# Kernel optimization log

Hardware: AMD Instinct MI355X
Metric: run time of the kernel (lower is better)

The kernel has to match this reference:

```python
import jax, jax.numpy as jnp
import numpy as np

HEADS = 4


def rel_to_abs(x):
    """Convert relative logits [..., L, 2L-1] to absolute [..., L, L].
    out[..., i, j] = x[..., i, j - i + L - 1]."""
    L = x.shape[-2]
    idx = jnp.arange(L)[None, :] - jnp.arange(L)[:, None] + (L - 1)  # [L, L]
    idx = jnp.broadcast_to(idx, x.shape[:-1] + (L,))
    return jnp.take_along_axis(x, idx, axis=-1)


def setup_inputs() -> dict:
    key = jax.random.key(0)
    ks = jax.random.split(key, 5)
    b, c, h, w = 2, 256, 64, 64
    dh = c // HEADS
    return {
        "x": jax.random.normal(ks[0], (b, c, h, w), jnp.float32),
        "w_qkv": jax.random.normal(ks[1], (3 * c, c), jnp.float32) / np.float32(np.sqrt(c)),
        "w_out": jax.random.normal(ks[2], (c, c), jnp.float32) / np.float32(np.sqrt(c)),
        "rel_height": jax.random.normal(ks[3], (2 * h - 1, dh), jnp.float32),
        "rel_width": jax.random.normal(ks[4], (2 * w - 1, dh), jnp.float32),
    }


def reference(x, w_qkv, w_out, rel_height, rel_width):
    b, c, h, w = x.shape
    dh = c // HEADS
    N = h * w
    scale = dh ** -0.5

    # 1x1 conv == per-pixel matmul over channels
    qkv = jnp.einsum('bchw,oc->bohw', x, w_qkv)  # [b, 3c, h, w]
    q, k, v = jnp.split(qkv, 3, axis=1)

    def to_heads(t):  # [b, c, h, w] -> [b, H, N, dh]
        return t.reshape(b, HEADS, dh, N).transpose(0, 1, 3, 2)

    q = to_heads(q) * scale
    k = to_heads(k)
    v = to_heads(v)

    # content-content scores over spatial positions
    content = jnp.einsum('bnid,bnjd->bnij', q, k)  # [b, H, N, N]

    q5 = q.reshape(b, HEADS, h, w, dh)  # [b, H, x, y, dh]
    # width relative logits: [b,H,x,y,2w-1] -> abs -> [b,H,x,y,jw]
    rw = rel_to_abs(jnp.einsum('bnxyd,rd->bnxyr', q5, rel_width))
    # height relative logits on transposed spatial: [b,H,y,x,2h-1] -> [b,H,y,x,jh]
    rh = rel_to_abs(jnp.einsum('bnyxd,rd->bnyxr', q5.transpose(0, 1, 3, 2, 4), rel_height))

    logits = content.reshape(b, HEADS, h, w, h, w)
    logits = logits + rw[:, :, :, :, None, :]  # broadcast width bias over target height jh
    logits = logits + rh.transpose(0, 1, 3, 2, 4)[:, :, :, :, :, None]  # [b,H,x,y,jh] over jw

    attn = jax.nn.softmax(logits.reshape(b, HEADS, N, N), axis=-1)
    out = jnp.einsum('bnij,bnjd->bnid', attn, v)  # [b, H, N, dh]
    out = out.transpose(0, 1, 3, 2).reshape(b, c, h, w)
    out = jnp.einsum('bchw,oc->bohw', out, w_out)  # 1x1 out projection
    return out + x
```

## Files before the change

kernel.cpp:

```cpp
#include <hip/hip_runtime.h>

typedef unsigned short u16;
typedef unsigned int u32;
typedef __bf16 bf16x8 __attribute__((ext_vector_type(8)));
typedef __bf16 bf16x2 __attribute__((ext_vector_type(2)));
typedef float f32x4 __attribute__((ext_vector_type(4)));
typedef float f32x2 __attribute__((ext_vector_type(2)));
typedef u32 u32x4 __attribute__((ext_vector_type(4)));
typedef u32 u32x2 __attribute__((ext_vector_type(2)));
typedef short s16x4 __attribute__((ext_vector_type(4)));

#define DEVI __device__ __forceinline__

#if defined(__has_builtin)
#if __has_builtin(__builtin_amdgcn_exp2f)
#define EXP2F(x) __builtin_amdgcn_exp2f(x)
#endif
#endif
#ifndef EXP2F
#define EXP2F(x) exp2f(x)
#endif

#define MFMA16(a, b, c) __builtin_amdgcn_mfma_f32_16x16x32_bf16(a, b, c, 0, 0, 0)
#define MFMA1K(a, b, c) __builtin_amdgcn_mfma_f32_16x16x16bf16_1k(a, b, c, 0, 0, 0)

typedef __attribute__((address_space(1))) u32 gu32;
typedef __attribute__((address_space(3))) u32 lu32;
DEVI void gll16(const u16* g, u16* l) {
    __builtin_amdgcn_global_load_lds((const gu32*)g, (lu32*)l, 16, 0, 0);
}
#define WAIT_VM0() __builtin_amdgcn_s_waitcnt(0x0f70)

DEVI u16 f2bf(float f) {
    u32 u = __builtin_bit_cast(u32, f);
    u = (u + 0x7FFFu + ((u >> 16) & 1u)) >> 16;
    return (u16)u;
}
DEVI float bf2f(u16 h) {
    u32 u = ((u32)h) << 16;
    return __builtin_bit_cast(float, u);
}
DEVI float bfhi(u32 u) { return __builtin_bit_cast(float, u & 0xFFFF0000u); }
DEVI float bflo(u32 u) { return __builtin_bit_cast(float, u << 16); }
DEVI bf16x8 bc8(u32x4 u) { return __builtin_bit_cast(bf16x8, u); }
DEVI s16x4 bc4(u32 a, u32 b) {
    u32x2 v = {a, b};
    return __builtin_bit_cast(s16x4, v);
}
DEVI u32 pack2(float a, float b) {
    f32x2 v = {a, b};
    bf16x2 h = __builtin_convertvector(v, bf16x2);
    return __builtin_bit_cast(u32, h);
}

#define QSCALE 0.18033688011112042f

__global__ __launch_bounds__(256) void k_prep(const float* __restrict__ x,
                                              const float* __restrict__ wq,
                                              const float* __restrict__ wo,
                                              const float* __restrict__ relh,
                                              const float* __restrict__ relw,
                                              u16* __restrict__ xt, u16* __restrict__ wqb,
                                              u16* __restrict__ wob, u16* __restrict__ relhb,
                                              u16* __restrict__ relwb) {
    int bid = blockIdx.x;
    int t = threadIdx.x;
    if (bid < 512) {
        int pm = bid & 63, cm = (bid >> 6) & 3, b = bid >> 8;
        int p0 = pm * 64, c0 = cm * 64;
        __shared__ float tile[64][65];
#pragma unroll
        for (int it = 0; it < 4; ++it) {
            int idx = it * 256 + t;
            int cl = idx >> 4, f4 = idx & 15;
            f32x4 v = *(const f32x4*)(x + ((size_t)(b * 256 + c0 + cl)) * 4096 + p0 + f4 * 4);
            tile[cl][f4 * 4 + 0] = v[0];
            tile[cl][f4 * 4 + 1] = v[1];
            tile[cl][f4 * 4 + 2] = v[2];
            tile[cl][f4 * 4 + 3] = v[3];
        }
        __syncthreads();
#pragma unroll
        for (int it = 0; it < 2; ++it) {
            int idx = it * 256 + t;
            int pl = idx >> 3, g = idx & 7;
            u32x4 pk;
            pk.x = pack2(tile[g * 8 + 0][pl], tile[g * 8 + 1][pl]);
            pk.y = pack2(tile[g * 8 + 2][pl], tile[g * 8 + 3][pl]);
            pk.z = pack2(tile[g * 8 + 4][pl], tile[g * 8 + 5][pl]);
            pk.w = pack2(tile[g * 8 + 6][pl], tile[g * 8 + 7][pl]);
            *(u32x4*)(xt + ((size_t)(b * 4096 + p0 + pl)) * 256 + c0 + g * 8) = pk;
        }
    } else {
        int i0 = (bid - 512) * 256 + t;
#pragma unroll
        for (int i = i0; i < 196608; i += 65536) wqb[i] = f2bf(wq[i]);
        if (i0 < 65536) wob[i0] = f2bf(wo[i0]);
        if (i0 < 8192) {
            relhb[i0] = (i0 < 8128) ? f2bf(relh[i0]) : (u16)0;
            relwb[i0] = (i0 < 8128) ? f2bf(relw[i0]) : (u16)0;
        }
    }
}

__global__ __launch_bounds__(256) void k_qkv(const u16* __restrict__ xt, const u16* __restrict__ wqb,
                                             const u16* __restrict__ relwb,
                                             const u16* __restrict__ relhb,
                                             u16* __restrict__ q, u16* __restrict__ k,
                                             u16* __restrict__ vt, u16* __restrict__ Wabs,
                                             u16* __restrict__ HabsT) {
    int pm = blockIdx.x, on = blockIdx.y, b = blockIdx.z;
    int p0 = pm * 64, o0 = on * 64;
    __shared__ __align__(16) u16 Sm[64 * 256];
    int t = threadIdx.x;
    int wv = t >> 6, l = t & 63, quad = l >> 4, li = l & 15;

    u32x4 areg[8];
    const u32x4* arow = (const u32x4*)(xt + ((size_t)(b * 4096 + p0 + wv * 16 + li)) * 256);
#pragma unroll
    for (int kc = 0; kc < 8; ++kc) areg[kc] = arow[kc * 4 + quad];

    {
        int pc = l & 31;
#pragma unroll
        for (int i = 0; i < 8; ++i) {
            int r = wv * 16 + i * 2 + (l >> 5);
            gll16(wqb + (size_t)(o0 + r) * 256 + ((pc + r) & 31) * 8,
                  Sm + (wv * 16 + i * 2) * 256);
        }
    }
    WAIT_VM0();
    __syncthreads();

    f32x4 acc[4] = {{0, 0, 0, 0}, {0, 0, 0, 0}, {0, 0, 0, 0}, {0, 0, 0, 0}};
#pragma unroll
    for (int kc = 0; kc < 8; ++kc) {
        bf16x8 a = bc8(areg[kc]);
#pragma unroll
        for (int ct = 0; ct < 4; ++ct) {
            bf16x8 bb = bc8(*(const u32x4*)(Sm + (ct * 16 + li) * 256 +
                                            (((kc * 4 + quad) - (ct * 16 + li)) & 31) * 8));
            acc[ct] = MFMA16(a, bb, acc[ct]);
        }
    }

    int tensor = on >> 2, head = on & 3;
    if (tensor == 2) {
        __syncthreads();
        u16* T = Sm;
#pragma unroll
        for (int ct = 0; ct < 4; ++ct)
#pragma unroll
            for (int r = 0; r < 4; ++r)
                T[(ct * 16 + li) * 72 + wv * 16 + quad * 4 + r] = f2bf(acc[ct][r]);
        __syncthreads();
        int dr = t >> 2, pc = (t & 3) * 16;
        u32x4* g = (u32x4*)(vt + ((size_t)((b * 4 + head) * 64 + dr)) * 4096 + p0 + pc);
        const u32x4* s2 = (const u32x4*)(T + dr * 72 + pc);
        g[0] = s2[0];
        g[1] = s2[1];
    } else {
        u16* outp = (tensor == 0) ? q : k;
        float sc = (tensor == 0) ? QSCALE : 1.0f;
#pragma unroll
        for (int ct = 0; ct < 4; ++ct)
#pragma unroll
            for (int r = 0; r < 4; ++r) {
                int p = p0 + wv * 16 + quad * 4 + r;
                int d = ct * 16 + li;
                outp[((size_t)((b * 4 + head) * 4096 + p)) * 64 + d] = f2bf(acc[ct][r] * sc);
            }
        if (tensor == 0) {
            int bh = b * 4 + head;
            u16* T = Sm;
            u16* Ls = Sm + 64 * 72;
            __syncthreads();
#pragma unroll
            for (int ct = 0; ct < 4; ++ct)
#pragma unroll
                for (int r = 0; r < 4; ++r)
                    T[(wv * 16 + quad * 4 + r) * 72 + ct * 16 + li] = f2bf(acc[ct][r] * QSCALE);
            {
                int row = t >> 1, half = t & 1;
                const u32x4* g2 = (const u32x4*)(relwb + row * 64 + half * 32);
                u32x4* s2 = (u32x4*)(Ls + row * 72 + half * 32);
#pragma unroll
                for (int kk = 0; kk < 4; ++kk) s2[kk] = g2[kk];
            }
            __syncthreads();
            u32x4 aq2[2];
            aq2[0] = *(const u32x4*)(T + (wv * 16 + li) * 72 + quad * 8);
            aq2[1] = *(const u32x4*)(T + (wv * 16 + li) * 72 + 32 + quad * 8);

            f32x4 acc2[8];
#pragma unroll
            for (int ct = 0; ct < 8; ++ct) acc2[ct] = (f32x4){0.f, 0.f, 0.f, 0.f};
#pragma unroll
            for (int kc = 0; kc < 2; ++kc) {
                bf16x8 a = bc8(aq2[kc]);
#pragma unroll
                for (int ct = 0; ct < 8; ++ct) {
                    bf16x8 bb = bc8(*(const u32x4*)(Ls + (ct * 16 + li) * 72 + kc * 32 + quad * 8));
                    acc2[ct] = MFMA16(a, bb, acc2[ct]);
                }
            }
#pragma unroll
            for (int ct = 0; ct < 8; ++ct)
#pragma unroll
                for (int r = 0; r < 4; ++r) {
                    int row = wv * 16 + quad * 4 + r;
                    int j = (ct * 16 + li) - 63 + row;
                    if (j >= 0 && j < 64)
                        Wabs[((size_t)(bh * 4096 + p0 + row)) * 64 + j] = f2bf(acc2[ct][r]);
                }
            __syncthreads();
            {
                int row = t >> 1, half = t & 1;
                const u32x4* g2 = (const u32x4*)(relhb + row * 64 + half * 32);
                u32x4* s2 = (u32x4*)(Ls + row * 72 + half * 32);
#pragma unroll
                for (int kk = 0; kk < 4; ++kk) s2[kk] = g2[kk];
            }
            __syncthreads();
#pragma unroll
            for (int ct = 0; ct < 8; ++ct) acc2[ct] = (f32x4){0.f, 0.f, 0.f, 0.f};
#pragma unroll
            for (int kc = 0; kc < 2; ++kc) {
                bf16x8 a = bc8(aq2[kc]);
#pragma unroll
                for (int ct = 0; ct < 8; ++ct) {
                    bf16x8 bb = bc8(*(const u32x4*)(Ls + (ct * 16 + li) * 72 + kc * 32 + quad * 8));
                    acc2[ct] = MFMA16(a, bb, acc2[ct]);
                }
            }
#pragma unroll
            for (int ct = 0; ct < 8; ++ct)
#pragma unroll
                for (int r = 0; r < 4; ++r) {
                    int row = wv * 16 + quad * 4 + r;
                    int j = (ct * 16 + li) - 63 + pm;
                    if (j >= 0 && j < 64)
                        HabsT[((size_t)(bh * 64 + j)) * 4096 + p0 + row] = f2bf(acc2[ct][r]);
                }
        }
    }
}

__global__ __launch_bounds__(256, 2) void k_flash(const u16* __restrict__ q,
                                                  const u16* __restrict__ kg,
                                                  const u16* __restrict__ vt,
                                                  const u16* __restrict__ Wabs,
                                                  const u16* __restrict__ HabsT,
                                                  u16* __restrict__ OP,
                                                  float* __restrict__ LS) {
    int pm = blockIdx.x, bh = blockIdx.y, ks = blockIdx.z;
    int p0 = pm * 128;
    __shared__ __align__(16) u16 Kt[2][64 * 72];
    __shared__ __align__(16) u16 Vl[2][64 * 72];
    int t = threadIdx.x, wv = t >> 6, l = t & 63, quad = l >> 4, li = l & 15;
    int rbase = wv * 32;

    u32x4 aq[2][2];
#pragma unroll
    for (int rs = 0; rs < 2; ++rs) {
        const u32x4* qrow =
            (const u32x4*)(q + ((size_t)(bh * 4096 + p0 + rbase + rs * 16 + li)) * 64);
        aq[rs][0] = qrow[quad];
        aq[rs][1] = qrow[4 + quad];
    }

    f32x4 wb4[2][4];
#pragma unroll
    for (int rs = 0; rs < 2; ++rs)
#pragma unroll
        for (int ct = 0; ct < 4; ++ct) {
            const u32* wp = (const u32*)(Wabs +
                                         ((size_t)(bh * 4096 + p0 + rbase + rs * 16 + li)) * 64 +
                                         ct * 16 + quad * 4);
            u32 lo = wp[0], hi = wp[1];
            wb4[rs][ct] = (f32x4){bflo(lo), bfhi(lo), bflo(hi), bfhi(hi)};
        }

    const u16* hbase = HabsT + ((size_t)(bh * 64 + ks * 32)) * 4096 + p0 + rbase;

    int srow = t >> 2, scc = (t & 3) * 16, jt4 = (t & 3) * 4;
    {
        int j0 = ks * 2048;
        const u32x4* gk = (const u32x4*)(kg + ((size_t)(bh * 4096 + j0 + srow)) * 64 + scc);
        u32x4* sk = (u32x4*)(Kt[0] + srow * 72 + scc);
        sk[0] = gk[0];
        sk[1] = gk[1];
        const u32x4* gv = (const u32x4*)(vt + ((size_t)(bh * 64 + srow)) * 4096 + j0 + scc);
        u32x4 v0 = gv[0], v1 = gv[1];
        u16* vr = Vl[0] + srow * 72;
        *(u32x2*)(vr + jt4) = (u32x2){v0.x, v0.y};
        *(u32x2*)(vr + 16 + jt4) = (u32x2){v0.z, v0.w};
        *(u32x2*)(vr + 32 + jt4) = (u32x2){v1.x, v1.y};
        *(u32x2*)(vr + 48 + jt4) = (u32x2){v1.z, v1.w};
    }
    u16 hc0 = hbase[li];
    u16 hc1 = hbase[16 + li];

    f32x4 oacc[2][5];
#pragma unroll
    for (int rs = 0; rs < 2; ++rs)
#pragma unroll
        for (int ct = 0; ct < 5; ++ct) oacc[rs][ct] = (f32x4){0.f, 0.f, 0.f, 0.f};

    const s16x4 ones = {(short)0x3F80, (short)0x3F80, (short)0x3F80, (short)0x3F80};

    u32x4 kreg[2], vreg[2];
    u16 hn0, hn1;
    for (int kt = 0; kt < 32; ++kt) {
        __syncthreads();
        int cur = kt & 1;
        const u16* Kc = Kt[cur];
        const u16* Vc = Vl[cur];
        if (kt < 31) {
            int j0 = (ks * 32 + kt + 1) * 64;
            const u32x4* gk = (const u32x4*)(kg + ((size_t)(bh * 4096 + j0 + srow)) * 64 + scc);
            kreg[0] = gk[0];
            kreg[1] = gk[1];
            const u32x4* gv = (const u32x4*)(vt + ((size_t)(bh * 64 + srow)) * 4096 + j0 + scc);
            vreg[0] = gv[0];
            vreg[1] = gv[1];
            hn0 = hbase[(size_t)(kt + 1) * 4096 + li];
            hn1 = hbase[(size_t)(kt + 1) * 4096 + 16 + li];
        }

        float hh0 = bf2f(hc0);
        float hh1 = bf2f(hc1);
        f32x4 s[2][4];
#pragma unroll
        for (int ct = 0; ct < 4; ++ct) {
            s[0][ct] = wb4[0][ct] + hh0;
            s[1][ct] = wb4[1][ct] + hh1;
        }
#pragma unroll
        for (int kc = 0; kc < 2; ++kc) {
            bf16x8 b0 = bc8(aq[0][kc]), b1 = bc8(aq[1][kc]);
#pragma unroll
            for (int ct = 0; ct < 4; ++ct) {
                bf16x8 af = bc8(*(const u32x4*)(Kc + (ct * 16 + li) * 72 + kc * 32 + quad * 8));
                s[0][ct] = MFMA16(af, b0, s[0][ct]);
                s[1][ct] = MFMA16(af, b1, s[1][ct]);
            }
        }

        s16x4 pf[2][4];
#pragma unroll
        for (int rs = 0; rs < 2; ++rs)
#pragma unroll
            for (int ct = 0; ct < 4; ++ct) {
                u32x2 pp;
                pp.x = pack2(EXP2F(s[rs][ct][0]), EXP2F(s[rs][ct][1]));
                pp.y = pack2(EXP2F(s[rs][ct][2]), EXP2F(s[rs][ct][3]));
                pf[rs][ct] = __builtin_bit_cast(s16x4, pp);
            }

#pragma unroll
        for (int dt = 0; dt < 4; ++dt) {
            const u16* vr = Vc + (dt * 16 + li) * 72 + quad * 16;
            u32x4 B0 = *(const u32x4*)(vr);
            u32x4 B1 = *(const u32x4*)(vr + 8);
            s16x4 bv0 = bc4(B0.x, B0.y), bv1 = bc4(B0.z, B0.w);
            s16x4 bv2 = bc4(B1.x, B1.y), bv3 = bc4(B1.z, B1.w);
            oacc[0][dt] = MFMA1K(pf[0][0], bv0, oacc[0][dt]);
            oacc[1][dt] = MFMA1K(pf[1][0], bv0, oacc[1][dt]);
            oacc[0][dt] = MFMA1K(pf[0][1], bv1, oacc[0][dt]);
            oacc[1][dt] = MFMA1K(pf[1][1], bv1, oacc[1][dt]);
            oacc[0][dt] = MFMA1K(pf[0][2], bv2, oacc[0][dt]);
            oacc[1][dt] = MFMA1K(pf[1][2], bv2, oacc[1][dt]);
            oacc[0][dt] = MFMA1K(pf[0][3], bv3, oacc[0][dt]);
            oacc[1][dt] = MFMA1K(pf[1][3], bv3, oacc[1][dt]);
        }
#pragma unroll
        for (int jt = 0; jt < 4; ++jt) {
            oacc[0][4] = MFMA1K(pf[0][jt], ones, oacc[0][4]);
            oacc[1][4] = MFMA1K(pf[1][jt], ones, oacc[1][4]);
        }

        if (kt < 31) {
            u32x4* sk = (u32x4*)(Kt[cur ^ 1] + srow * 72 + scc);
            sk[0] = kreg[0];
            sk[1] = kreg[1];
            u16* vr = Vl[cur ^ 1] + srow * 72;
            *(u32x2*)(vr + jt4) = (u32x2){vreg[0].x, vreg[0].y};
            *(u32x2*)(vr + 16 + jt4) = (u32x2){vreg[0].z, vreg[0].w};
            *(u32x2*)(vr + 32 + jt4) = (u32x2){vreg[1].x, vreg[1].y};
            *(u32x2*)(vr + 48 + jt4) = (u32x2){vreg[1].z, vreg[1].w};
            hc0 = hn0;
            hc1 = hn1;
        }
    }

#pragma unroll
    for (int rs = 0; rs < 2; ++rs) {
#pragma unroll
        for (int ct = 0; ct < 4; ++ct)
#pragma unroll
            for (int r = 0; r < 4; ++r) {
                int p = p0 + rbase + rs * 16 + quad * 4 + r;
                OP[((size_t)((ks * 8 + bh) * 4096 + p)) * 64 + ct * 16 + li] =
                    f2bf(oacc[rs][ct][r]);
            }
        if (li == 0) {
#pragma unroll
            for (int r = 0; r < 4; ++r) {
                int p = p0 + rbase + rs * 16 + quad * 4 + r;
                LS[(size_t)(ks * 8 + bh) * 4096 + p] = oacc[rs][4][r];
            }
        }
    }
}

__global__ __launch_bounds__(256) void k_out2(const u16* __restrict__ wob,
                                              const u16* __restrict__ OP,
                                              const float* __restrict__ LS,
                                              const float* __restrict__ x,
                                              float* __restrict__ out) {
    int pm = blockIdx.x, b = blockIdx.y, coh = blockIdx.z;
    int p0 = pm * 64;
    __shared__ __align__(16) u16 Bt[64 * 264];
    int t = threadIdx.x, wv = t >> 6, l = t & 63, quad = l >> 4, li = l & 15;

    {
        int row = t >> 2, head = t & 3;
        int bh = b * 4 + head;
        int p = p0 + row;
        const u32x4* o0p = (const u32x4*)(OP + ((size_t)(bh * 4096 + p)) * 64);
        const u32x4* o1p = (const u32x4*)(OP + ((size_t)((8 + bh) * 4096 + p)) * 64);
        float linv = 1.0f / (LS[(size_t)bh * 4096 + p] + LS[(size_t)(8 + bh) * 4096 + p]);
        u16* dst = Bt + row * 264 + head * 64;
#pragma unroll
        for (int kk = 0; kk < 8; ++kk) {
            u32x4 a = o0p[kk], c = o1p[kk];
            u32x4 pk;
            pk.x = pack2((bflo(a.x) + bflo(c.x)) * linv, (bfhi(a.x) + bfhi(c.x)) * linv);
            pk.y = pack2((bflo(a.y) + bflo(c.y)) * linv, (bfhi(a.y) + bfhi(c.y)) * linv);
            pk.z = pack2((bflo(a.z) + bflo(c.z)) * linv, (bfhi(a.z) + bfhi(c.z)) * linv);
            pk.w = pack2((bflo(a.w) + bflo(c.w)) * linv, (bfhi(a.w) + bfhi(c.w)) * linv);
            *(u32x4*)(dst + kk * 8) = pk;
        }
    }
    __syncthreads();

#pragma unroll
    for (int ci = 0; ci < 2; ++ci) {
        int com = coh * 2 + ci;
        int co0 = com * 64;
        f32x4 acc[4] = {{0, 0, 0, 0}, {0, 0, 0, 0}, {0, 0, 0, 0}, {0, 0, 0, 0}};
        const u32x4* arow = (const u32x4*)(wob + (size_t)(co0 + wv * 16 + li) * 256);
#pragma unroll
        for (int kc = 0; kc < 8; ++kc) {
            bf16x8 a = bc8(arow[kc * 4 + quad]);
#pragma unroll
            for (int ct = 0; ct < 4; ++ct) {
                bf16x8 bb = bc8(*(const u32x4*)(Bt + (ct * 16 + li) * 264 + kc * 32 + quad * 8));
                acc[ct] = MFMA16(a, bb, acc[ct]);
            }
        }
#pragma unroll
        for (int ct = 0; ct < 4; ++ct)
#pragma unroll
            for (int r = 0; r < 4; ++r) {
                size_t idx =
                    ((size_t)(b * 256 + co0 + wv * 16 + quad * 4 + r)) * 4096 + p0 + ct * 16 + li;
                out[idx] = acc[ct][r] + x[idx];
            }
    }
}

extern "C" void kernel_launch(void* const* d_in, const int* in_sizes, int n_in, void* d_out,
                              int out_size, void* d_ws, size_t ws_size, hipStream_t stream) {
    const float* x = (const float*)d_in[0];
    const float* wqkv = (const float*)d_in[1];
    const float* wout = (const float*)d_in[2];
    const float* relh = (const float*)d_in[3];
    const float* relw = (const float*)d_in[4];
    float* out = (float*)d_out;
    char* ws = (char*)d_ws;

    u16* xt = (u16*)(ws + 0);
    u16* wqb = (u16*)(ws + 4194304);
    u16* wob = (u16*)(ws + 4587520);
    u16* relwb = (u16*)(ws + 4718592);
    u16* relhb = (u16*)(ws + 4734976);
    u16* qb = (u16*)(ws + 4751360);
    u16* kb = (u16*)(ws + 8945664);
    u16* vtb = (u16*)(ws + 13139968);
    u16* Wabs = (u16*)(ws + 17334272);
    u16* HabsT = (u16*)(ws + 21528576);
    u16* OPart = (u16*)(ws + 25722880);
    float* LSum = (float*)(ws + 0);

    k_prep<<<768, 256, 0, stream>>>(x, wqkv, wout, relh, relw, xt, wqb, wob, relhb, relwb);
    k_qkv<<<dim3(64, 12, 2), 256, 0, stream>>>(xt, wqb, relwb, relhb, qb, kb, vtb, Wabs, HabsT);
    k_flash<<<dim3(32, 8, 2), 256, 0, stream>>>(qb, kb, vtb, Wabs, HabsT, OPart, LSum);
    k_out2<<<dim3(64, 2, 2), 256, 0, stream>>>(wob, OPart, LSum, x, out);
}
```

Measured before the change: 147.2 us.

## Drop split-K in flash kernel and normalize output in-kernel

Removes the two-way split over key blocks in the flash attention kernel, so each block walks all 64 key tiles and normalizes its output by the row sum before writing. The out-projection kernel then copies normalized output straight into shared memory instead of merging two partials and sum buffers. This cuts partial-result traffic and merge arithmetic, but halves the flash grid to 256 blocks, which lowers parallelism on a GPU with many CUs.

```diff
diff --git a/kernel.cpp b/kernel.cpp
--- a/kernel.cpp
+++ b/kernel.cpp
@@ -251,9 +251,8 @@
                                                   const u16* __restrict__ vt,
                                                   const u16* __restrict__ Wabs,
                                                   const u16* __restrict__ HabsT,
-                                                  u16* __restrict__ OP,
-                                                  float* __restrict__ LS) {
-    int pm = blockIdx.x, bh = blockIdx.y, ks = blockIdx.z;
+                                                  u16* __restrict__ O) {
+    int pm = blockIdx.x, bh = blockIdx.y;
     int p0 = pm * 128;
     __shared__ __align__(16) u16 Kt[2][64 * 72];
     __shared__ __align__(16) u16 Vl[2][64 * 72];
@@ -281,16 +280,15 @@
             wb4[rs][ct] = (f32x4){bflo(lo), bfhi(lo), bflo(hi), bfhi(hi)};
         }
 
-    const u16* hbase = HabsT + ((size_t)(bh * 64 + ks * 32)) * 4096 + p0 + rbase;
+    const u16* hbase = HabsT + ((size_t)(bh * 64)) * 4096 + p0 + rbase;
 
     int srow = t >> 2, scc = (t & 3) * 16, jt4 = (t & 3) * 4;
     {
-        int j0 = ks * 2048;
-        const u32x4* gk = (const u32x4*)(kg + ((size_t)(bh * 4096 + j0 + srow)) * 64 + scc);
+        const u32x4* gk = (const u32x4*)(kg + ((size_t)(bh * 4096 + srow)) * 64 + scc);
         u32x4* sk = (u32x4*)(Kt[0] + srow * 72 + scc);
         sk[0] = gk[0];
         sk[1] = gk[1];
-        const u32x4* gv = (const u32x4*)(vt + ((size_t)(bh * 64 + srow)) * 4096 + j0 + scc);
+        const u32x4* gv = (const u32x4*)(vt + ((size_t)(bh * 64 + srow)) * 4096 + scc);
         u32x4 v0 = gv[0], v1 = gv[1];
         u16* vr = Vl[0] + srow * 72;
         *(u32x2*)(vr + jt4) = (u32x2){v0.x, v0.y};
@@ -311,13 +309,13 @@
 
     u32x4 kreg[2], vreg[2];
     u16 hn0, hn1;
-    for (int kt = 0; kt < 32; ++kt) {
+    for (int kt = 0; kt < 64; ++kt) {
         __syncthreads();
         int cur = kt & 1;
         const u16* Kc = Kt[cur];
         const u16* Vc = Vl[cur];
-        if (kt < 31) {
-            int j0 = (ks * 32 + kt + 1) * 64;
+        if (kt < 63) {
+            int j0 = (kt + 1) * 64;
             const u32x4* gk = (const u32x4*)(kg + ((size_t)(bh * 4096 + j0 + srow)) * 64 + scc);
             kreg[0] = gk[0];
             kreg[1] = gk[1];
@@ -380,7 +378,7 @@
             oacc[1][4] = MFMA1K(pf[1][jt], ones, oacc[1][4]);
         }
 
-        if (kt < 31) {
+        if (kt < 63) {
             u32x4* sk = (u32x4*)(Kt[cur ^ 1] + srow * 72 + scc);
             sk[0] = kreg[0];
             sk[1] = kreg[1];
@@ -396,27 +394,22 @@
 
 #pragma unroll
     for (int rs = 0; rs < 2; ++rs) {
+        float linv[4];
+#pragma unroll
+        for (int r = 0; r < 4; ++r) linv[r] = 1.0f / oacc[rs][4][r];
 #pragma unroll
         for (int ct = 0; ct < 4; ++ct)
 #pragma unroll
             for (int r = 0; r < 4; ++r) {
                 int p = p0 + rbase + rs * 16 + quad * 4 + r;
-                OP[((size_t)((ks * 8 + bh) * 4096 + p)) * 64 + ct * 16 + li] =
-                    f2bf(oacc[rs][ct][r]);
-            }
-        if (li == 0) {
-#pragma unroll
-            for (int r = 0; r < 4; ++r) {
-                int p = p0 + rbase + rs * 16 + quad * 4 + r;
-                LS[(size_t)(ks * 8 + bh) * 4096 + p] = oacc[rs][4][r];
-            }
-        }
+                O[((size_t)(bh * 4096 + p)) * 64 + ct * 16 + li] =
+                    f2bf(oacc[rs][ct][r] * linv[r]);
+            }
     }
 }
 
 __global__ __launch_bounds__(256) void k_out2(const u16* __restrict__ wob,
-                                              const u16* __restrict__ OP,
-                                              const float* __restrict__ LS,
+                                              const u16* __restrict__ O,
                                               const float* __restrict__ x,
                                               float* __restrict__ out) {
     int pm = blockIdx.x, b = blockIdx.y, coh = blockIdx.z;
@@ -426,22 +419,10 @@
 
     {
         int row = t >> 2, head = t & 3;
-        int bh = b * 4 + head;
-        int p = p0 + row;
-        const u32x4* o0p = (const u32x4*)(OP + ((size_t)(bh * 4096 + p)) * 64);
-        const u32x4* o1p = (const u32x4*)(OP + ((size_t)((8 + bh) * 4096 + p)) * 64);
-        float linv = 1.0f / (LS[(size_t)bh * 4096 + p] + LS[(size_t)(8 + bh) * 4096 + p]);
-        u16* dst = Bt + row * 264 + head * 64;
-#pragma unroll
-        for (int kk = 0; kk < 8; ++kk) {
-            u32x4 a = o0p[kk], c = o1p[kk];
-            u32x4 pk;
-            pk.x = pack2((bflo(a.x) + bflo(c.x)) * linv, (bfhi(a.x) + bfhi(c.x)) * linv);
-            pk.y = pack2((bflo(a.y) + bflo(c.y)) * linv, (bfhi(a.y) + bfhi(c.y)) * linv);
-            pk.z = pack2((bflo(a.z) + bflo(c.z)) * linv, (bfhi(a.z) + bfhi(c.z)) * linv);
-            pk.w = pack2((bflo(a.w) + bflo(c.w)) * linv, (bfhi(a.w) + bfhi(c.w)) * linv);
-            *(u32x4*)(dst + kk * 8) = pk;
-        }
+        const u32x4* src = (const u32x4*)(O + ((size_t)((b * 4 + head) * 4096 + p0 + row)) * 64);
+        u32x4* dst = (u32x4*)(Bt + row * 264 + head * 64);
+#pragma unroll
+        for (int kk = 0; kk < 8; ++kk) dst[kk] = src[kk];
     }
     __syncthreads();
 
@@ -491,11 +472,10 @@
     u16* vtb = (u16*)(ws + 13139968);
     u16* Wabs = (u16*)(ws + 17334272);
     u16* HabsT = (u16*)(ws + 21528576);
-    u16* OPart = (u16*)(ws + 25722880);
-    float* LSum = (float*)(ws + 0);
+    u16* Ob = xt;
 
     k_prep<<<768, 256, 0, stream>>>(x, wqkv, wout, relh, relw, xt, wqb, wob, relhb, relwb);
     k_qkv<<<dim3(64, 12, 2), 256, 0, stream>>>(xt, wqb, relwb, relhb, qb, kb, vtb, Wabs, HabsT);
-    k_flash<<<dim3(32, 8, 2), 256, 0, stream>>>(qb, kb, vtb, Wabs, HabsT, OPart, LSum);
-    k_out2<<<dim3(64, 2, 2), 256, 0, stream>>>(wob, OPart, LSum, x, out);
-}
+    k_flash<<<dim3(32, 8), 256, 0, stream>>>(qb, kb, vtb, Wabs, HabsT, Ob);
+    k_out2<<<dim3(64, 2, 2), 256, 0, stream>>>(wob, Ob, x, out);
+}
```

Result: slower. 162.7 us (+10.6%).
